# Optimization experiments

Measured on AMD Instinct MI355X. Metric: run time of the kernel, lower is better.

## Reference

```python
import jax, jax.numpy as jnp
import numpy as np

B, S, I = 64, 32, 64
N_ITEMS = 100000
E, H = 256, 128


def setup_inputs() -> dict:
    key = jax.random.key(0)
    k_len, k_ids, k_ut, k_emb, k_wih, k_whh, k_a1, k_a2, k_vt = jax.random.split(key, 9)
    n_sess = B * S
    # ragged session lengths in [2, I] -> trailing zero padding, all sessions valid
    lengths = jax.random.randint(k_len, (n_sess,), 2, I + 1)
    ids = jax.random.randint(k_ids, (n_sess, I), 1, N_ITEMS + 1)
    pad_mask = jnp.arange(I)[None, :] < lengths[:, None]
    item_id = (ids * pad_mask).reshape(B, S, I).astype(jnp.int32)
    eval_from = jnp.zeros((B,), dtype=jnp.int32)
    u_type = jax.random.randint(k_ut, (B,), 0, 5).astype(jnp.int32)
    sc = 0.05
    emb = jax.random.normal(k_emb, (N_ITEMS + 1, E), jnp.float32) * sc
    emb = emb.at[0].set(0.0)  # padding_idx=0
    W_ih = jax.random.normal(k_wih, (3 * H, E), jnp.float32) * sc
    W_hh = jax.random.normal(k_whh, (3 * H, H), jnp.float32) * sc
    b_ih = jnp.zeros((3 * H,), jnp.float32)
    b_hh = jnp.zeros((3 * H,), jnp.float32)
    W_a1 = jax.random.normal(k_a1, (H, H), jnp.float32) * sc
    W_a2 = jax.random.normal(k_a2, (H, H), jnp.float32) * sc
    W_vt = jax.random.normal(k_vt, (1, H), jnp.float32) * sc
    return {"item_id": item_id, "eval_from": eval_from, "u_type": u_type,
            "emb": emb, "W_ih": W_ih, "W_hh": W_hh, "b_ih": b_ih, "b_hh": b_hh,
            "W_a1": W_a1, "W_a2": W_a2, "W_vt": W_vt}


def _gru(x, lengths, W_ih, W_hh, b_ih, b_hh):
    # x: [L, N, E]; packed-GRU semantics: state frozen past each length,
    # outputs zero at padded steps (matches pad_packed_sequence).
    L, N, _ = x.shape
    Hh = W_hh.shape[1]

    def step(h, inp):
        xt, t = inp
        gi = xt @ W_ih.T + b_ih           # [N, 3H]
        gh = h @ W_hh.T + b_hh
        i_r, i_z, i_n = jnp.split(gi, 3, axis=-1)
        h_r, h_z, h_n = jnp.split(gh, 3, axis=-1)
        r = jax.nn.sigmoid(i_r + h_r)
        z = jax.nn.sigmoid(i_z + h_z)
        n = jnp.tanh(i_n + r * h_n)
        h_new = (1.0 - z) * n + z * h
        valid = (t < lengths)[:, None]
        h_next = jnp.where(valid, h_new, h)
        out = jnp.where(valid, h_new, 0.0)
        return h_next, out

    h0 = jnp.zeros((N, Hh), x.dtype)
    hT, outs = jax.lax.scan(step, h0, (x, jnp.arange(L)))
    return outs, hT  # outs: [L, N, H], hT: [N, H]


def reference(item_id, eval_from, u_type, emb, W_ih, W_hh, b_ih, b_hh, W_a1, W_a2, W_vt):
    b, s, i = item_id.shape
    ids = jnp.clip(item_id, 0)
    allow = jnp.arange(s)[None, :] >= eval_from[:, None]        # [B, S]
    ids = ids * allow[:, :, None].astype(ids.dtype)
    sess = ids.reshape(b * s, i)                                # [N, I]
    lengths = (sess != 0).sum(1)                                # all >= 2 by construction
    n = sess.shape[0]
    target = sess[jnp.arange(n), lengths - 1]
    len_in = lengths - 1
    L = i - 1  # static L_in_max; extra padded steps are masked out
    mask = (jnp.arange(L)[None, :] < len_in[:, None])           # [N, L]
    inp = sess[:, :L] * mask.astype(sess.dtype)
    x = emb[inp]                                                # [N, L, E] (dropout=identity, eval)
    outs, ht = _gru(x.transpose(1, 0, 2), len_in, W_ih, W_hh, b_ih, b_hh)
    gru = outs.transpose(1, 0, 2)                               # [N, L, H]
    q1 = jnp.einsum('nlh,kh->nlk', gru, W_a1)
    q2 = (ht @ W_a2.T)[:, None, :]
    alpha = jnp.einsum('nlh,oh->nlo', jax.nn.sigmoid(q1 + q2), W_vt)[..., 0] * mask
    c_loc = jnp.einsum('nl,nlh->nh', alpha, gru)
    reps = jnp.concatenate([c_loc, ht], axis=1)                 # [N, 2H] (ct dropout=identity)
    u = jnp.repeat(u_type, s)
    return reps, target, u
```

## Files before the change

kernel.cpp:

```cpp
#include <hip/hip_runtime.h>
#include <hip/hip_bf16.h>

#define NSESS 2048
#define NI 64
#define LL 63
#define EE 256
#define HH 128
#define GG 384

typedef __attribute__((ext_vector_type(8))) short short8;
typedef __attribute__((ext_vector_type(4))) float f32x4;

static __device__ __forceinline__ unsigned short f2b(float f) {
  union { float f; unsigned u; } v; v.f = f;
  unsigned r = (v.u + 0x7FFFu + ((v.u >> 16) & 1u)) >> 16;
  return (unsigned short)r;
}
static __device__ __forceinline__ float b2f(unsigned short s) {
  union { unsigned u; float f; } v; v.u = ((unsigned)s) << 16;
  return v.f;
}
static __device__ __forceinline__ float sigmoidf_(float x) {
  return 1.f / (1.f + __expf(-x));
}
static __device__ __forceinline__ float tanh2_(float y) {
  float e = __expf(2.f * y);
  return 1.f - 2.f / (1.f + e);
}
static __device__ __forceinline__ void barrier_lds_only() {
  asm volatile("s_waitcnt lgkmcnt(0)" ::: "memory");
  __builtin_amdgcn_sched_barrier(0);
  __builtin_amdgcn_s_barrier();
  __builtin_amdgcn_sched_barrier(0);
}

__global__ __launch_bounds__(64) void prep_kernel(const int* __restrict__ item_id,
                                                  const int* __restrict__ eval_from,
                                                  const int* __restrict__ u_type,
                                                  int* __restrict__ len_in,
                                                  int* __restrict__ inp,
                                                  float* __restrict__ out) {
  int n = blockIdx.x;
  int lane = threadIdx.x;
  int b = n >> 5, s = n & 31;
  int allow = (s >= eval_from[b]) ? 1 : 0;
  int id = item_id[n * NI + lane];
  if (id < 0) id = 0;
  id *= allow;
  unsigned long long m = __ballot(id != 0);
  int length = __popcll(m);
  int li = length - 1;
  int tv = __shfl(id, (length > 0) ? (length - 1) : 0, 64);
  int target = (length > 0) ? tv : 0;
  if (lane < LL) inp[n * LL + lane] = (lane < li) ? id : 0;
  if (lane == 0) {
    len_in[n] = li;
    out[NSESS * 256 + n] = (float)target;
    out[NSESS * 256 + NSESS + n] = (float)u_type[b];
  }
}

__global__ __launch_bounds__(256) void cvt_weights(const float* __restrict__ W_ih,
                                                   const float* __restrict__ W_hh,
                                                   const float* __restrict__ W_a1,
                                                   unsigned short* __restrict__ Wb,
                                                   unsigned short* __restrict__ Whs,
                                                   unsigned short* __restrict__ Wa1b) {
  int i = blockIdx.x * 256 + threadIdx.x;
  Wb[i] = f2b(W_ih[i]);
  if (i < GG * HH) Whs[i] = f2b(W_hh[i]);
  if (i < HH * HH) Wa1b[i] = f2b(W_a1[i]);
}

__global__ __launch_bounds__(512, 2) void gemm_in(const float* __restrict__ emb,
                                                  const unsigned short* __restrict__ Wb,
                                                  const float* __restrict__ b_ih,
                                                  const int* __restrict__ inp,
                                                  unsigned short* __restrict__ gi) {
  constexpr int XP = 264;
  __shared__ unsigned short Ash[2][16 * XP];

  const int t = threadIdx.x;
  const int lane = t & 63, w = t >> 6;
  const int ccol = lane & 15, kg = lane >> 4;
  const int g0 = w * 48;

  short8 bfr[3][8];
#pragma unroll
  for (int nt = 0; nt < 3; ++nt) {
    const unsigned short* wrow = Wb + (long)(g0 + nt * 16 + ccol) * EE + kg * 8;
#pragma unroll
    for (int c = 0; c < 8; ++c) bfr[nt][c] = *(const short8*)(wrow + c * 32);
  }
  float bias[3];
#pragma unroll
  for (int nt = 0; nt < 3; ++nt) bias[nt] = b_ih[g0 + nt * 16 + ccol];

  const int tile0 = blockIdx.x * 8;
  const int srow = t >> 5;
  const int scol = (t & 31) * 8;

  {
    long rid = inp[tile0 * 16 + srow];
    const float* x = emb + rid * EE + scol;
    float4 a0 = *(const float4*)x, a1 = *(const float4*)(x + 4);
    short8 v;
    v[0]=(short)f2b(a0.x); v[1]=(short)f2b(a0.y); v[2]=(short)f2b(a0.z); v[3]=(short)f2b(a0.w);
    v[4]=(short)f2b(a1.x); v[5]=(short)f2b(a1.y); v[6]=(short)f2b(a1.z); v[7]=(short)f2b(a1.w);
    *(short8*)(&Ash[0][srow * XP + scol]) = v;
  }
  __syncthreads();

  for (int i = 0; i < 8; ++i) {
    const int cur = i & 1;
    const int m0 = (tile0 + i) * 16;

    float4 a0, a1;
    if (i + 1 < 8) {
      long rid = inp[(tile0 + i + 1) * 16 + srow];
      const float* x = emb + rid * EE + scol;
      a0 = *(const float4*)x; a1 = *(const float4*)(x + 4);
    }

    f32x4 acc[3];
#pragma unroll
    for (int nt = 0; nt < 3; ++nt)
      acc[nt] = (f32x4){bias[nt], bias[nt], bias[nt], bias[nt]};
#pragma unroll
    for (int c = 0; c < 8; ++c) {
      short8 af = *(const short8*)(&Ash[cur][ccol * XP + c * 32 + kg * 8]);
#pragma unroll
      for (int nt = 0; nt < 3; ++nt)
        acc[nt] = __builtin_amdgcn_mfma_f32_16x16x32_bf16(af, bfr[nt][c], acc[nt], 0, 0, 0);
    }

    long base[4];
#pragma unroll
    for (int j = 0; j < 4; ++j) {
      int m = m0 + kg * 4 + j;
      int n = m / 63;
      int l = m - 63 * n;
      base[j] = ((long)l * NSESS + n) * GG;
    }
#pragma unroll
    for (int nt = 0; nt < 3; ++nt) {
      int g = g0 + nt * 16 + ccol;
#pragma unroll
      for (int j = 0; j < 4; ++j)
        gi[base[j] + g] = f2b(acc[nt][j]);
    }

    if (i + 1 < 8) {
      short8 v;
      v[0]=(short)f2b(a0.x); v[1]=(short)f2b(a0.y); v[2]=(short)f2b(a0.z); v[3]=(short)f2b(a0.w);
      v[4]=(short)f2b(a1.x); v[5]=(short)f2b(a1.y); v[6]=(short)f2b(a1.z); v[7]=(short)f2b(a1.w);
      *(short8*)(&Ash[cur ^ 1][srow * XP + scol]) = v;
    }
    barrier_lds_only();
  }
}

__global__ __launch_bounds__(512) void gru_mfma(const unsigned short* __restrict__ Whs,
                                                const float* __restrict__ b_hh,
                                                const unsigned short* __restrict__ gi,
                                                const int* __restrict__ len_in,
                                                unsigned short* __restrict__ outs,
                                                float* __restrict__ ht,
                                                float* __restrict__ out) {
  __shared__ unsigned short ring[8 * 2048];
  __shared__ int lens_s[16];

  const int t = threadIdx.x;
  const int w = t >> 6, lane = t & 63;
  const int ccol = lane & 15, kg = lane >> 4;
  const int sbase = kg * 4;
  const int n0 = blockIdx.x * 16;
  const int jh = w * 16 + ccol;

  short8 bfr[3][4];
#pragma unroll
  for (int cls = 0; cls < 3; ++cls) {
    const unsigned short* wrow = Whs + (long)(cls * HH + jh) * HH;
#pragma unroll
    for (int c = 0; c < 4; ++c)
      bfr[cls][c] = *(const short8*)(wrow + c * 32 + kg * 8);
  }
  float bh[3];
#pragma unroll
  for (int cls = 0; cls < 3; ++cls) bh[cls] = b_hh[cls * HH + jh];

  int li[4];
#pragma unroll
  for (int r = 0; r < 4; ++r) li[r] = len_in[n0 + sbase + r];
  float hold[4] = {0.f, 0.f, 0.f, 0.f};

  for (int idx = t; idx < 8 * 2048; idx += 512) ring[idx] = 0;
  if (t < 16) lens_s[t] = len_in[n0 + t];

  const unsigned short* gbase = gi + (long)(n0 + sbase) * GG + jh;
  const long lstride = (long)NSESS * GG;
#define GADDR(l, cls, r) (gbase + (long)(l) * lstride + (r) * GG + (cls) * HH)

  unsigned short gA[12], gB[12];
#pragma unroll
  for (int k = 0; k < 12; ++k) gA[k] = *GADDR(0, k >> 2, k & 3);
#pragma unroll
  for (int k = 0; k < 12; ++k) gB[k] = *GADDR(1, k >> 2, k & 3);

  barrier_lds_only();

  for (int W = 0; W < 16; ++W) {
#pragma unroll
    for (int l2 = 0; l2 < 4; ++l2) {
      const int l = 4 * W + l2;
      if (l < LL) {
        float gvv[12];
        if ((l2 & 1) == 0) {
#pragma unroll
          for (int k = 0; k < 12; ++k) gvv[k] = b2f(gA[k]);
        } else {
#pragma unroll
          for (int k = 0; k < 12; ++k) gvv[k] = b2f(gB[k]);
        }
        if (l + 2 < LL) {
          if ((l2 & 1) == 0) {
#pragma unroll
            for (int k = 0; k < 12; ++k) gA[k] = *GADDR(l + 2, k >> 2, k & 3);
          } else {
#pragma unroll
            for (int k = 0; k < 12; ++k) gB[k] = *GADDR(l + 2, k >> 2, k & 3);
          }
        }

        const unsigned short* rb = ring + ((l + 7) & 7) * 2048 + ccol * HH;
        short8 af[4];
#pragma unroll
        for (int c = 0; c < 4; ++c)
          af[c] = *(const short8*)(rb + ((c * 32 + kg * 8) ^ ((ccol & 7) << 3)));

        f32x4 acc[3];
#pragma unroll
        for (int cls = 0; cls < 3; ++cls) {
          acc[cls] = (f32x4){bh[cls], bh[cls], bh[cls], bh[cls]};
#pragma unroll
          for (int c = 0; c < 4; ++c)
            acc[cls] = __builtin_amdgcn_mfma_f32_16x16x32_bf16(af[c], bfr[cls][c], acc[cls], 0, 0, 0);
        }

        unsigned short* wrb = ring + (l & 7) * 2048;
#pragma unroll
        for (int r = 0; r < 4; ++r) {
          float rg = sigmoidf_(gvv[0 * 4 + r] + acc[0][r]);
          float zg = sigmoidf_(gvv[1 * 4 + r] + acc[1][r]);
          float ng = tanh2_(gvv[2 * 4 + r] + rg * acc[2][r]);
          float hnew = ng + zg * (hold[r] - ng);
          hold[r] = (l < li[r]) ? hnew : hold[r];
          int sess = sbase + r;
          wrb[sess * HH + (jh ^ ((sess & 7) << 3))] = f2b(hold[r]);
        }
        barrier_lds_only();
      }
    }

#pragma unroll
    for (int half = 0; half < 2; ++half) {
      int idx = half * 512 + t;
      int dl2 = idx >> 8, sess = (idx >> 4) & 15, col8 = (idx & 15) * 8;
      int dl = 4 * W + dl2;
      if (dl < LL) {
        int slot = (W & 1) * 4 + dl2;
        short8 hv = *(const short8*)(ring + slot * 2048 + sess * HH +
                                     (col8 ^ ((sess & 7) << 3)));
        if (dl >= lens_s[sess]) hv = (short8){0, 0, 0, 0, 0, 0, 0, 0};
        *(short8*)(outs + ((long)(n0 + sess) * LL + dl) * HH + col8) = hv;
      }
    }
  }
#undef GADDR

#pragma unroll
  for (int r = 0; r < 4; ++r) {
    int n = n0 + sbase + r;
    ht[(long)n * HH + jh] = hold[r];
    out[(long)n * 256 + HH + jh] = hold[r];
  }
}

__global__ __launch_bounds__(256) void attn(const unsigned short* __restrict__ outs,
                                            const float* __restrict__ ht,
                                            const unsigned short* __restrict__ Wa1b,
                                            const float* __restrict__ W_a2,
                                            const float* __restrict__ W_vt,
                                            const int* __restrict__ len_in,
                                            float* __restrict__ out) {
  constexpr int OP = HH + 8;
  __shared__ unsigned short o_l[64 * OP];
  __shared__ float q2s[HH];
  __shared__ float wvt[HH];
  __shared__ float hts[HH];
  __shared__ float aw[4][64];
  __shared__ float alphas[64];

  const int n = blockIdx.x;
  const int t = threadIdx.x;
  const int lane = t & 63, wv = t >> 6;
  const int ccol = lane & 15, kg = lane >> 4;
  const int li = len_in[n];

  const unsigned* src = (const unsigned*)(outs + (long)n * LL * HH);
  for (int idx = t; idx < LL * 64; idx += 256) {
    int r = idx >> 6, c2 = idx & 63;
    ((unsigned*)(o_l + r * OP))[c2] = src[r * 64 + c2];
  }
  if (t < 64) ((unsigned*)(o_l + 63 * OP))[t] = 0;
  if (t < HH) { hts[t] = ht[(long)n * HH + t]; wvt[t] = W_vt[t]; }

  short8 bfr[2][4];
#pragma unroll
  for (int nt = 0; nt < 2; ++nt) {
    int G = wv * 32 + nt * 16 + ccol;
#pragma unroll
    for (int c = 0; c < 4; ++c)
      bfr[nt][c] = *(const short8*)(Wa1b + (long)G * HH + c * 32 + kg * 8);
  }
  __syncthreads();

  if (t < HH) {
    float a = 0.f;
    const float* w2 = W_a2 + t * HH;
    for (int k = 0; k < HH; ++k) a += hts[k] * w2[k];
    q2s[t] = a;
  }
  __syncthreads();

  f32x4 acc[4][2];
#pragma unroll
  for (int mt = 0; mt < 4; ++mt)
#pragma unroll
    for (int nt = 0; nt < 2; ++nt) acc[mt][nt] = (f32x4){0.f, 0.f, 0.f, 0.f};
#pragma unroll
  for (int mt = 0; mt < 4; ++mt) {
#pragma unroll
    for (int c = 0; c < 4; ++c) {
      short8 af = *(const short8*)(o_l + (mt * 16 + ccol) * OP + c * 32 + kg * 8);
#pragma unroll
      for (int nt = 0; nt < 2; ++nt)
        acc[mt][nt] = __builtin_amdgcn_mfma_f32_16x16x32_bf16(af, bfr[nt][c], acc[mt][nt], 0, 0, 0);
    }
  }

  float q2v[2], wvv[2];
#pragma unroll
  for (int nt = 0; nt < 2; ++nt) {
    int cg = wv * 32 + nt * 16 + ccol;
    q2v[nt] = q2s[cg]; wvv[nt] = wvt[cg];
  }
#pragma unroll
  for (int mt = 0; mt < 4; ++mt) {
    float part[4] = {0.f, 0.f, 0.f, 0.f};
#pragma unroll
    for (int nt = 0; nt < 2; ++nt)
#pragma unroll
      for (int j = 0; j < 4; ++j)
        part[j] += sigmoidf_(acc[mt][nt][j] + q2v[nt]) * wvv[nt];
#pragma unroll
    for (int j = 0; j < 4; ++j) {
#pragma unroll
      for (int off = 1; off < 16; off <<= 1)
        part[j] += __shfl_xor(part[j], off, 64);
    }
    if (ccol == 0) {
#pragma unroll
      for (int j = 0; j < 4; ++j) aw[wv][mt * 16 + kg * 4 + j] = part[j];
    }
  }
  __syncthreads();

  if (t < 64) {
    float s = aw[0][t] + aw[1][t] + aw[2][t] + aw[3][t];
    alphas[t] = (t < li) ? s : 0.f;
  }
  __syncthreads();

  if (t < HH) {
    float c = 0.f;
    for (int l = 0; l < LL; ++l) c = fmaf(alphas[l], b2f(o_l[l * OP + t]), c);
    out[(long)n * 256 + t] = c;
  }
}

extern "C" void kernel_launch(void* const* d_in, const int* in_sizes, int n_in,
                              void* d_out, int out_size, void* d_ws, size_t ws_size,
                              hipStream_t stream) {
  (void)in_sizes; (void)n_in; (void)out_size; (void)ws_size;
  const int* item_id   = (const int*)d_in[0];
  const int* eval_from = (const int*)d_in[1];
  const int* u_type    = (const int*)d_in[2];
  const float* emb     = (const float*)d_in[3];
  const float* W_ih    = (const float*)d_in[4];
  const float* W_hh    = (const float*)d_in[5];
  const float* b_ih    = (const float*)d_in[6];
  const float* b_hh    = (const float*)d_in[7];
  const float* W_a1    = (const float*)d_in[8];
  const float* W_a2    = (const float*)d_in[9];
  const float* W_vt    = (const float*)d_in[10];

  float* out = (float*)d_out;
  char* ws = (char*)d_ws;
  int* len_in           = (int*)(ws + 0);
  int* inp              = (int*)(ws + 8192);
  unsigned short* Wb    = (unsigned short*)(ws + 524288);
  unsigned short* Whs   = (unsigned short*)(ws + 720896);
  float* ht             = (float*)(ws + 819200);
  unsigned short* gi    = (unsigned short*)(ws + 1867776);
  unsigned short* outs  = (unsigned short*)(ws + 100958208);
  unsigned short* Wa1b  = (unsigned short*)(ws + 133988352);

  prep_kernel<<<NSESS, 64, 0, stream>>>(item_id, eval_from, u_type, len_in, inp, out);
  cvt_weights<<<384, 256, 0, stream>>>(W_ih, W_hh, W_a1, Wb, Whs, Wa1b);
  gemm_in<<<1008, 512, 0, stream>>>(emb, Wb, b_ih, inp, gi);
  gru_mfma<<<NSESS / 16, 512, 0, stream>>>(Whs, b_hh, gi, len_in, outs, ht, out);
  attn<<<NSESS, 512, 0, stream>>>(outs, ht, Wa1b, W_a2, W_vt, len_in, out);
}
```

Baseline: 163.0 us.

## Transpose GRU MFMA operands so each lane owns contiguous hidden columns

The recurrent MFMA swaps its A/B operands (weights as A, hidden state as B), so each lane holds four consecutive hidden units of one session instead of one unit across four sessions. Gate inputs are then loaded as packed uint2 vectors rather than twelve scalar bf16 loads, and bias is loaded as a vector. Outputs go straight to global memory from each step, which removes the 8-slot LDS ring and the periodic copy-out pass, leaving a 2-slot double buffer. This trades many narrow global stores issued every step for fewer LDS writes and a shorter per-step critical path.

New measurement: 139.8 us. -14.2%, faster.

```diff
diff --git a/kernel.cpp b/kernel.cpp
--- a/kernel.cpp
+++ b/kernel.cpp
@@ -19,6 +19,12 @@
 static __device__ __forceinline__ float b2f(unsigned short s) {
   union { unsigned u; float f; } v; v.u = ((unsigned)s) << 16;
   return v.f;
+}
+static __device__ __forceinline__ float lo16(unsigned u) {
+  union { unsigned v; float f; } x; x.v = u << 16; return x.f;
+}
+static __device__ __forceinline__ float hi16(unsigned u) {
+  union { unsigned v; float f; } x; x.v = u & 0xFFFF0000u; return x.f;
 }
 static __device__ __forceinline__ float sigmoidf_(float x) {
   return 1.f / (1.f + __expf(-x));
@@ -167,15 +173,15 @@
                                                 unsigned short* __restrict__ outs,
                                                 float* __restrict__ ht,
                                                 float* __restrict__ out) {
-  __shared__ unsigned short ring[8 * 2048];
-  __shared__ int lens_s[16];
+  __shared__ unsigned short ring[2 * 2048];
 
   const int t = threadIdx.x;
   const int w = t >> 6, lane = t & 63;
   const int ccol = lane & 15, kg = lane >> 4;
-  const int sbase = kg * 4;
   const int n0 = blockIdx.x * 16;
   const int jh = w * 16 + ccol;
+  const int p0 = w * 16 + kg * 4;
+  const int swz = (ccol & 7) << 3;
 
   short8 bfr[3][4];
 #pragma unroll
@@ -185,105 +191,83 @@
     for (int c = 0; c < 4; ++c)
       bfr[cls][c] = *(const short8*)(wrow + c * 32 + kg * 8);
   }
-  float bh[3];
-#pragma unroll
-  for (int cls = 0; cls < 3; ++cls) bh[cls] = b_hh[cls * HH + jh];
-
-  int li[4];
-#pragma unroll
-  for (int r = 0; r < 4; ++r) li[r] = len_in[n0 + sbase + r];
+  f32x4 bhv[3];
+#pragma unroll
+  for (int cls = 0; cls < 3; ++cls)
+    bhv[cls] = *(const f32x4*)(b_hh + cls * HH + p0);
+
+  const int li = len_in[n0 + ccol];
   float hold[4] = {0.f, 0.f, 0.f, 0.f};
 
-  for (int idx = t; idx < 8 * 2048; idx += 512) ring[idx] = 0;
-  if (t < 16) lens_s[t] = len_in[n0 + t];
-
-  const unsigned short* gbase = gi + (long)(n0 + sbase) * GG + jh;
+  for (int idx = t; idx < 2 * 2048; idx += 512) ring[idx] = 0;
+
+  const unsigned short* gbase = gi + (long)(n0 + ccol) * GG + p0;
   const long lstride = (long)NSESS * GG;
-#define GADDR(l, cls, r) (gbase + (long)(l) * lstride + (r) * GG + (cls) * HH)
-
-  unsigned short gA[12], gB[12];
-#pragma unroll
-  for (int k = 0; k < 12; ++k) gA[k] = *GADDR(0, k >> 2, k & 3);
-#pragma unroll
-  for (int k = 0; k < 12; ++k) gB[k] = *GADDR(1, k >> 2, k & 3);
+#define GA(l, cls) ((const uint2*)(gbase + (long)(l) * lstride + (cls) * HH))
+
+  uint2 gA[3], gB[3];
+#pragma unroll
+  for (int cls = 0; cls < 3; ++cls) gA[cls] = *GA(0, cls);
+#pragma unroll
+  for (int cls = 0; cls < 3; ++cls) gB[cls] = *GA(1, cls);
 
   barrier_lds_only();
 
-  for (int W = 0; W < 16; ++W) {
-#pragma unroll
-    for (int l2 = 0; l2 < 4; ++l2) {
-      const int l = 4 * W + l2;
-      if (l < LL) {
-        float gvv[12];
-        if ((l2 & 1) == 0) {
-#pragma unroll
-          for (int k = 0; k < 12; ++k) gvv[k] = b2f(gA[k]);
-        } else {
-#pragma unroll
-          for (int k = 0; k < 12; ++k) gvv[k] = b2f(gB[k]);
-        }
-        if (l + 2 < LL) {
-          if ((l2 & 1) == 0) {
-#pragma unroll
-            for (int k = 0; k < 12; ++k) gA[k] = *GADDR(l + 2, k >> 2, k & 3);
-          } else {
-#pragma unroll
-            for (int k = 0; k < 12; ++k) gB[k] = *GADDR(l + 2, k >> 2, k & 3);
-          }
-        }
-
-        const unsigned short* rb = ring + ((l + 7) & 7) * 2048 + ccol * HH;
-        short8 af[4];
-#pragma unroll
-        for (int c = 0; c < 4; ++c)
-          af[c] = *(const short8*)(rb + ((c * 32 + kg * 8) ^ ((ccol & 7) << 3)));
-
-        f32x4 acc[3];
-#pragma unroll
-        for (int cls = 0; cls < 3; ++cls) {
-          acc[cls] = (f32x4){bh[cls], bh[cls], bh[cls], bh[cls]};
-#pragma unroll
-          for (int c = 0; c < 4; ++c)
-            acc[cls] = __builtin_amdgcn_mfma_f32_16x16x32_bf16(af[c], bfr[cls][c], acc[cls], 0, 0, 0);
-        }
-
-        unsigned short* wrb = ring + (l & 7) * 2048;
-#pragma unroll
-        for (int r = 0; r < 4; ++r) {
-          float rg = sigmoidf_(gvv[0 * 4 + r] + acc[0][r]);
-          float zg = sigmoidf_(gvv[1 * 4 + r] + acc[1][r]);
-          float ng = tanh2_(gvv[2 * 4 + r] + rg * acc[2][r]);
-          float hnew = ng + zg * (hold[r] - ng);
-          hold[r] = (l < li[r]) ? hnew : hold[r];
-          int sess = sbase + r;
-          wrb[sess * HH + (jh ^ ((sess & 7) << 3))] = f2b(hold[r]);
-        }
-        barrier_lds_only();
-      }
-    }
-
-#pragma unroll
-    for (int half = 0; half < 2; ++half) {
-      int idx = half * 512 + t;
-      int dl2 = idx >> 8, sess = (idx >> 4) & 15, col8 = (idx & 15) * 8;
-      int dl = 4 * W + dl2;
-      if (dl < LL) {
-        int slot = (W & 1) * 4 + dl2;
-        short8 hv = *(const short8*)(ring + slot * 2048 + sess * HH +
-                                     (col8 ^ ((sess & 7) << 3)));
-        if (dl >= lens_s[sess]) hv = (short8){0, 0, 0, 0, 0, 0, 0, 0};
-        *(short8*)(outs + ((long)(n0 + sess) * LL + dl) * HH + col8) = hv;
-      }
-    }
-  }
-#undef GADDR
-
-#pragma unroll
-  for (int r = 0; r < 4; ++r) {
-    int n = n0 + sbase + r;
-    ht[(long)n * HH + jh] = hold[r];
-    out[(long)n * 256 + HH + jh] = hold[r];
-  }
+  auto step = [&](int l, uint2 (&gbuf)[3]) {
+    float gvv[3][4];
+#pragma unroll
+    for (int cls = 0; cls < 3; ++cls) {
+      gvv[cls][0] = lo16(gbuf[cls].x); gvv[cls][1] = hi16(gbuf[cls].x);
+      gvv[cls][2] = lo16(gbuf[cls].y); gvv[cls][3] = hi16(gbuf[cls].y);
+    }
+    if (l + 2 < LL) {
+#pragma unroll
+      for (int cls = 0; cls < 3; ++cls) gbuf[cls] = *GA(l + 2, cls);
+    }
+
+    const unsigned short* rb = ring + ((l + 1) & 1) * 2048 + ccol * HH;
+    short8 hf[4];
+#pragma unroll
+    for (int c = 0; c < 4; ++c)
+      hf[c] = *(const short8*)(rb + ((c * 32 + kg * 8) ^ swz));
+
+    f32x4 acc[3];
+#pragma unroll
+    for (int cls = 0; cls < 3; ++cls) {
+      acc[cls] = bhv[cls];
+#pragma unroll
+      for (int c = 0; c < 4; ++c)
+        acc[cls] = __builtin_amdgcn_mfma_f32_16x16x32_bf16(bfr[cls][c], hf[c], acc[cls], 0, 0, 0);
+    }
+
+    bool valid = (l < li);
+#pragma unroll
+    for (int j = 0; j < 4; ++j) {
+      float rg = sigmoidf_(gvv[0][j] + acc[0][j]);
+      float zg = sigmoidf_(gvv[1][j] + acc[1][j]);
+      float ng = tanh2_(gvv[2][j] + rg * acc[2][j]);
+      float hnew = ng + zg * (hold[j] - ng);
+      hold[j] = valid ? hnew : hold[j];
+    }
+    uint2 hp;
+    hp.x = (unsigned)f2b(hold[0]) | ((unsigned)f2b(hold[1]) << 16);
+    hp.y = (unsigned)f2b(hold[2]) | ((unsigned)f2b(hold[3]) << 16);
+    *(uint2*)(ring + (l & 1) * 2048 + ccol * HH + (((w * 16 + kg * 4)) ^ swz)) = hp;
+    uint2 ov = valid ? hp : (uint2){0u, 0u};
+    *(uint2*)(outs + ((long)(n0 + ccol) * LL + l) * HH + p0) = ov;
+    barrier_lds_only();
+  };
+
+  for (int b2 = 0; b2 < 31; ++b2) {
+    step(2 * b2, gA);
+    step(2 * b2 + 1, gB);
+  }
+  step(62, gA);
+#undef GA
+
+  f32x4 hv = {hold[0], hold[1], hold[2], hold[3]};
+  *(f32x4*)(ht + (long)(n0 + ccol) * HH + p0) = hv;
+  *(f32x4*)(out + (long)(n0 + ccol) * 256 + HH + p0) = hv;
 }
 
 __global__ __launch_bounds__(256) void attn(const unsigned short* __restrict__ outs,
```
